# Kernel optimization log

Hardware: AMD Instinct MI355X
Metric: run time of the kernel (lower is better)

Reference implementation:

```python
import jax, jax.numpy as jnp
import numpy as np

B, F, T, K = 16, 256, 2048, 20
TEMP = 0.5
EPS = 1e-8  # torch cosine_similarity eps


def setup_inputs() -> dict:
    key = jax.random.key(0)
    k1, k2, k3 = jax.random.split(key, 3)
    z = jax.random.normal(k1, (B, F, T), dtype=jnp.float32)
    c = jax.random.normal(k2, (B, F, T + 1), dtype=jnp.float32)
    # torch: torch.randint(0, full_len - 1, size=(B, T * K))  -> values in [0, T-2]
    negative_inds = jax.random.randint(k3, (B, T * K), 0, T - 1, dtype=jnp.int64)
    return {"z": z, "c": c, "negative_inds": negative_inds}


def reference(z, c, negative_inds):
    # ---- _generate_negatives ----
    # z: [B, F, T] -> flat rows [B*T, F]
    z_flat = jnp.transpose(z, (0, 2, 1)).reshape(-1, F)
    # per-batch offset i*T (torch adds it in-place for i in 1..B-1)
    inds = negative_inds + (jnp.arange(B, dtype=negative_inds.dtype) * T)[:, None]
    negatives = z_flat[inds.reshape(-1)].reshape(B, T, K, F)

    # ---- _calculate_similarity ----
    c_t = jnp.transpose(c[..., 1:], (0, 2, 1))[:, :, None, :]  # [B, T, 1, F] (drop start token)
    z_t = jnp.transpose(z, (0, 2, 1))[:, :, None, :]           # [B, T, 1, F]
    neg_is_pos = jnp.all(c_t == negatives, axis=-1)            # [B, T, K]
    targets = jnp.concatenate([c_t, negatives], axis=-2)       # [B, T, K+1, F]

    num = jnp.sum(z_t * targets, axis=-1)                      # [B, T, K+1]
    denom = jnp.maximum(
        jnp.linalg.norm(z_t, axis=-1) * jnp.linalg.norm(targets, axis=-1), EPS
    )
    logits = (num / denom) / TEMP                              # [B, T, K+1]

    # mask negatives that exactly equal the positive (wav2vec2-style)
    pad = jnp.zeros_like(neg_is_pos[..., :1])
    full_mask = jnp.concatenate([pad, neg_is_pos], axis=-1)    # [B, T, K+1]
    logits = jnp.where(full_mask, -jnp.inf, logits)

    return logits.reshape(-1, K + 1)                           # [B*T, K+1]
```

## Files before the change

kernel.cpp:

```cpp
#include <hip/hip_runtime.h>
#include <hip/hip_fp16.h>
#include <math.h>

#define B_ 16
#define F_ 256
#define T_ 2048
#define K_ 20
#define OUTK 21
#define NPAIR 11
#define CTOFF (B_ * T_ * F_ * 2)

typedef _Float16 half2v __attribute__((ext_vector_type(2)));

__device__ __forceinline__ half2v h2(unsigned u) { return __builtin_bit_cast(half2v, u); }
__device__ __forceinline__ float fdot2f(unsigned a, unsigned b, float c) {
#if __has_builtin(__builtin_amdgcn_fdot2)
    return __builtin_amdgcn_fdot2(h2(a), h2(b), c, false);
#else
    half2v x = h2(a), y = h2(b);
    return fmaf((float)x[1], (float)y[1], fmaf((float)x[0], (float)y[0], c));
#endif
}

__global__ __launch_bounds__(256) void transpose_norm2_kernel(
    const float* __restrict__ z, const float* __restrict__ c,
    ushort* __restrict__ zth, ushort* __restrict__ cth,
    float* __restrict__ snz, float* __restrict__ snc)
{
    __shared__ float tile[256][33];
    int which = blockIdx.z;
    const float* src = which ? c : z;
    ushort* dst = which ? cth : zth;
    float* nrm = which ? snc : snz;
    int Lsrc = which ? (T_ + 1) : T_;
    int co   = which;

    int b  = blockIdx.y;
    int t0 = blockIdx.x * 32;
    const float* srcb = src + (size_t)b * F_ * Lsrc;
    int tl = threadIdx.x & 31;
    int fl = threadIdx.x >> 5;
#pragma unroll
    for (int i = 0; i < 32; ++i) {
        int f = i * 8 + fl;
        tile[f][tl] = srcb[(size_t)f * Lsrc + (t0 + tl + co)];
    }
    __syncthreads();
    int l   = threadIdx.x & 127;
    int rhi = threadIdx.x >> 7;
#pragma unroll
    for (int j2 = 0; j2 < 16; ++j2) {
        int row = j2 * 2 + rhi;
        float a  = tile[2 * l][row];
        float bb = tile[2 * l + 1][row];
        unsigned u = ((unsigned)__half_as_ushort(__float2half(bb)) << 16)
                   |  (unsigned)__half_as_ushort(__float2half(a));
        unsigned* drow = (unsigned*)(dst + ((size_t)b * T_ + t0 + row) * F_);
        drow[l] = u;
    }
    if (threadIdx.x < 32) {
        float s = 0.f;
#pragma unroll 8
        for (int f = 0; f < 256; ++f) { float v = tile[f][threadIdx.x]; s += v * v; }
        nrm[b * T_ + t0 + threadIdx.x] = sqrtf(s);
    }
}

__device__ __forceinline__ float dpp_half_sum(float x) {
    x += __int_as_float(__builtin_amdgcn_mov_dpp(__float_as_int(x), 0x111, 0xF, 0xF, true));
    x += __int_as_float(__builtin_amdgcn_mov_dpp(__float_as_int(x), 0x112, 0xF, 0xF, true));
    x += __int_as_float(__builtin_amdgcn_mov_dpp(__float_as_int(x), 0x114, 0xF, 0xF, true));
    x += __int_as_float(__builtin_amdgcn_mov_dpp(__float_as_int(x), 0x118, 0xF, 0xF, true));
    x += __int_as_float(__builtin_amdgcn_mov_dpp(__float_as_int(x), 0x142, 0xF, 0xF, true));
    return x;
}

__global__ __launch_bounds__(256, 4) void sim_kernel(
    const ushort* __restrict__ zth, const ushort* __restrict__ cth,
    const float* __restrict__ snz, const float* __restrict__ snc,
    const int* __restrict__ inds, float* __restrict__ out)
{
    __shared__ float sd[128];
    int i = blockIdx.x;
    int b = (i & 7) | ((i >= 4096) ? 8 : 0);
    int wid = threadIdx.x >> 6;
    int t = (((i >> 3) & 511) << 2) + wid;
    int lane = threadIdx.x & 63;
    int hl = lane & 31;
    int hi = lane >> 5;
    int bt = __builtin_amdgcn_readfirstlane((b << 11) + t);

    const int* myinds = inds + bt * K_;
    int idxv = myinds[(lane < K_) ? lane : 0];
    int lm1 = (lane >= 1 && lane <= K_) ? (lane - 1) : 0;
    int myidx = myinds[lm1];
    const float* np = (lane == 0) ? (snc + bt)
                    : ((lane <= K_) ? (snz + ((b << 11) + myidx)) : (snz + bt));
    float stn = *np;
    float szn = snz[bt];

    const uint4* zrow = (const uint4*)(zth + (size_t)bt * F_);
    const uint4* crow = (const uint4*)(cth + (size_t)bt * F_);
    uint4 zv = zrow[hl];
    uint4 cv = crow[hl];

    const char* tbl = (const char*)zth;
    unsigned base_z  = (unsigned)(b << 11) * 512u;
    unsigned laneoff = (unsigned)hl * 16u;

    uint4 tv[NPAIR];
    {
        unsigned olo = (unsigned)CTOFF + (unsigned)bt * 512u;
        unsigned ohi = base_z + (unsigned)__builtin_amdgcn_readlane(idxv, 0) * 512u;
        tv[0] = *(const uint4*)(tbl + ((hi ? ohi : olo) + laneoff));
    }
#pragma unroll
    for (int p = 1; p < NPAIR; ++p) {
        unsigned ilo = (unsigned)__builtin_amdgcn_readlane(idxv, 2 * p - 1);
        unsigned ihi = (unsigned)__builtin_amdgcn_readlane(idxv, (p == 10) ? 19 : 2 * p);
        unsigned off = base_z + (hi ? ihi : ilo) * 512u + laneoff;
        tv[p] = *(const uint4*)(tbl + off);
    }

    __builtin_amdgcn_sched_barrier(0);

    float dz[NPAIR];
#pragma unroll
    for (int p = 0; p < NPAIR; ++p) {
        float d = fdot2f(tv[p].x, zv.x, 0.f);
        d = fdot2f(tv[p].y, zv.y, d);
        d = fdot2f(tv[p].z, zv.z, d);
        d = fdot2f(tv[p].w, zv.w, d);
        dz[p] = d;
    }

    unsigned mb = 0;
#pragma unroll
    for (int p = 0; p < NPAIR; ++p) {
        unsigned long long ball = __ballot(tv[p].x == cv.x);
        unsigned blo = (unsigned)ball, bhi = (unsigned)(ball >> 32);
        if (blo == 0xFFFFFFFFu || bhi == 0xFFFFFFFFu) {
            bool full = (tv[p].x == cv.x) && (tv[p].y == cv.y) &&
                        (tv[p].z == cv.z) && (tv[p].w == cv.w);
            unsigned long long b2 = __ballot(full);
            if ((unsigned)b2 == 0xFFFFFFFFu)          mb |= 1u << (2 * p);
            if ((unsigned)(b2 >> 32) == 0xFFFFFFFFu)  mb |= 1u << (2 * p + 1);
        }
    }
    mb &= ~1u;

#pragma unroll
    for (int p = 0; p < NPAIR; ++p) dz[p] = dpp_half_sum(dz[p]);

    int slotbase = wid * 32 + hi;
    if (hl == 31) {
#pragma unroll
        for (int p = 0; p < NPAIR; ++p) sd[slotbase + 2 * p] = dz[p];
    }

    if (lane < OUTK) {
        float d = sd[wid * 32 + lane];
        float den = fmaxf(szn * stn, 1e-8f);
        float v = (d / den) * 2.0f;
        if ((mb >> lane) & 1u) v = -INFINITY;
        out[(size_t)bt * OUTK + lane] = v;
    }
}

extern "C" void kernel_launch(void* const* d_in, const int* in_sizes, int n_in,
                              void* d_out, int out_size, void* d_ws, size_t ws_size,
                              hipStream_t stream)
{
    const float* z    = (const float*)d_in[0];
    const float* c    = (const float*)d_in[1];
    const int*   inds = (const int*)d_in[2];
    float* out = (float*)d_out;

    char* ws = (char*)d_ws;
    size_t th_bytes = (size_t)B_ * T_ * F_ * sizeof(ushort);
    ushort* zth = (ushort*)ws;
    ushort* cth = (ushort*)(ws + th_bytes);
    float*  snz = (float*)(ws + 2 * th_bytes);
    float*  snc = snz + B_ * T_;

    dim3 tb(256), tg(T_ / 32, B_, 2);
    transpose_norm2_kernel<<<tg, tb, 0, stream>>>(z, c, zth, cth, snz, snc);
    sim_kernel<<<dim3(B_ * T_ / 4), dim3(256), 0, stream>>>(zth, cth, snz, snc, inds, out);
}
```

Baseline: 47.47 us.

## Compute per-row dot products with MFMA 16x16x32 instead of fdot2 plus DPP reduction

Replaces the per-lane fdot2 dot products, DPP cross-lane reduction and LDS staging with two MFMA 16x16x32 f16 ops per K-slice. The anchor z row is replicated as the A operand and 16+5 target rows form the B columns, so each result comes out directly in the accumulator. The equality mask is now built with a cheap first-chunk check and a full compare only when a candidate matches. The A operand re-reads the same row eight times per wave, most of the MFMA output is wasted, and register pressure grows, so the occupancy hint drops from 4 to 3.

```diff
diff --git a/kernel.cpp b/kernel.cpp
--- a/kernel.cpp
+++ b/kernel.cpp
@@ -7,20 +7,10 @@
 #define T_ 2048
 #define K_ 20
 #define OUTK 21
-#define NPAIR 11
 #define CTOFF (B_ * T_ * F_ * 2)
 
-typedef _Float16 half2v __attribute__((ext_vector_type(2)));
-
-__device__ __forceinline__ half2v h2(unsigned u) { return __builtin_bit_cast(half2v, u); }
-__device__ __forceinline__ float fdot2f(unsigned a, unsigned b, float c) {
-#if __has_builtin(__builtin_amdgcn_fdot2)
-    return __builtin_amdgcn_fdot2(h2(a), h2(b), c, false);
-#else
-    half2v x = h2(a), y = h2(b);
-    return fmaf((float)x[1], (float)y[1], fmaf((float)x[0], (float)y[0], c));
-#endif
-}
+typedef _Float16 half8 __attribute__((ext_vector_type(8)));
+typedef float f32x4 __attribute__((ext_vector_type(4)));
 
 __global__ __launch_bounds__(256) void transpose_norm2_kernel(
     const float* __restrict__ z, const float* __restrict__ c,
@@ -66,32 +56,30 @@
     }
 }
 
-__device__ __forceinline__ float dpp_half_sum(float x) {
-    x += __int_as_float(__builtin_amdgcn_mov_dpp(__float_as_int(x), 0x111, 0xF, 0xF, true));
-    x += __int_as_float(__builtin_amdgcn_mov_dpp(__float_as_int(x), 0x112, 0xF, 0xF, true));
-    x += __int_as_float(__builtin_amdgcn_mov_dpp(__float_as_int(x), 0x114, 0xF, 0xF, true));
-    x += __int_as_float(__builtin_amdgcn_mov_dpp(__float_as_int(x), 0x118, 0xF, 0xF, true));
-    x += __int_as_float(__builtin_amdgcn_mov_dpp(__float_as_int(x), 0x142, 0xF, 0xF, true));
-    return x;
+__device__ __forceinline__ unsigned fold16(unsigned long long x) {
+    return (unsigned)(x & 0xFFFFu) & (unsigned)((x >> 16) & 0xFFFFu)
+         & (unsigned)((x >> 32) & 0xFFFFu) & (unsigned)(x >> 48);
+}
+__device__ __forceinline__ bool eq16(uint4 a, uint4 b) {
+    return (a.x == b.x) && (a.y == b.y) && (a.z == b.z) && (a.w == b.w);
 }
 
-__global__ __launch_bounds__(256, 4) void sim_kernel(
+__global__ __launch_bounds__(256, 3) void sim_kernel(
     const ushort* __restrict__ zth, const ushort* __restrict__ cth,
     const float* __restrict__ snz, const float* __restrict__ snc,
     const int* __restrict__ inds, float* __restrict__ out)
 {
-    __shared__ float sd[128];
     int i = blockIdx.x;
     int b = (i & 7) | ((i >= 4096) ? 8 : 0);
     int wid = threadIdx.x >> 6;
     int t = (((i >> 3) & 511) << 2) + wid;
     int lane = threadIdx.x & 63;
-    int hl = lane & 31;
-    int hi = lane >> 5;
+    int slot = lane & 15;
+    int kg = lane >> 4;
     int bt = __builtin_amdgcn_readfirstlane((b << 11) + t);
 
     const int* myinds = inds + bt * K_;
-    int idxv = myinds[(lane < K_) ? lane : 0];
+
     int lm1 = (lane >= 1 && lane <= K_) ? (lane - 1) : 0;
     int myidx = myinds[lm1];
     const float* np = (lane == 0) ? (snc + bt)
@@ -99,67 +87,61 @@
     float stn = *np;
     float szn = snz[bt];
 
-    const uint4* zrow = (const uint4*)(zth + (size_t)bt * F_);
-    const uint4* crow = (const uint4*)(cth + (size_t)bt * F_);
-    uint4 zv = zrow[hl];
-    uint4 cv = crow[hl];
+    int i0 = myinds[(slot >= 1) ? (slot - 1) : 0];
+    int i1 = myinds[(slot <= 4) ? (15 + slot) : 19];
+    unsigned zbase = (unsigned)(b << 11) * 512u;
+    unsigned cbyte = (unsigned)CTOFF + (unsigned)bt * 512u;
+    unsigned rb0 = (slot == 0) ? cbyte : (zbase + (unsigned)i0 * 512u);
+    unsigned rb1 = zbase + (unsigned)i1 * 512u;
+    unsigned qoff = (unsigned)kg * 16u;
+    unsigned abase = (unsigned)bt * 512u;
 
     const char* tbl = (const char*)zth;
-    unsigned base_z  = (unsigned)(b << 11) * 512u;
-    unsigned laneoff = (unsigned)hl * 16u;
 
-    uint4 tv[NPAIR];
-    {
-        unsigned olo = (unsigned)CTOFF + (unsigned)bt * 512u;
-        unsigned ohi = base_z + (unsigned)__builtin_amdgcn_readlane(idxv, 0) * 512u;
-        tv[0] = *(const uint4*)(tbl + ((hi ? ohi : olo) + laneoff));
+    uint4 Bf0[8], Bf1[8], Af[8], c0;
+#pragma unroll
+    for (int s = 0; s < 8; ++s) {
+        Bf0[s] = *(const uint4*)(tbl + rb0 + 64u * s + qoff);
+        Bf1[s] = *(const uint4*)(tbl + rb1 + 64u * s + qoff);
+        Af[s]  = *(const uint4*)(tbl + abase + 64u * s + qoff);
     }
-#pragma unroll
-    for (int p = 1; p < NPAIR; ++p) {
-        unsigned ilo = (unsigned)__builtin_amdgcn_readlane(idxv, 2 * p - 1);
-        unsigned ihi = (unsigned)__builtin_amdgcn_readlane(idxv, (p == 10) ? 19 : 2 * p);
-        unsigned off = base_z + (hi ? ihi : ilo) * 512u + laneoff;
-        tv[p] = *(const uint4*)(tbl + off);
-    }
+    c0 = *(const uint4*)(tbl + cbyte + qoff);
 
     __builtin_amdgcn_sched_barrier(0);
 
-    float dz[NPAIR];
+    f32x4 acc0 = {0.f, 0.f, 0.f, 0.f};
+    f32x4 acc1 = {0.f, 0.f, 0.f, 0.f};
 #pragma unroll
-    for (int p = 0; p < NPAIR; ++p) {
-        float d = fdot2f(tv[p].x, zv.x, 0.f);
-        d = fdot2f(tv[p].y, zv.y, d);
-        d = fdot2f(tv[p].z, zv.z, d);
-        d = fdot2f(tv[p].w, zv.w, d);
-        dz[p] = d;
+    for (int s = 0; s < 8; ++s) {
+        half8 a = __builtin_bit_cast(half8, Af[s]);
+        acc0 = __builtin_amdgcn_mfma_f32_16x16x32_f16(
+                   a, __builtin_bit_cast(half8, Bf0[s]), acc0, 0, 0, 0);
+        acc1 = __builtin_amdgcn_mfma_f32_16x16x32_f16(
+                   a, __builtin_bit_cast(half8, Bf1[s]), acc1, 0, 0, 0);
     }
 
+    bool e0 = eq16(Bf0[0], c0);
+    bool e1 = eq16(Bf1[0], c0);
+    unsigned m0 = fold16(__ballot(e0)) & 0xFFFEu;
+    unsigned m1 = fold16(__ballot(e1)) & 0x001Fu;
     unsigned mb = 0;
+    if (m0 | m1) {
+        bool f0 = e0, f1 = e1;
 #pragma unroll
-    for (int p = 0; p < NPAIR; ++p) {
-        unsigned long long ball = __ballot(tv[p].x == cv.x);
-        unsigned blo = (unsigned)ball, bhi = (unsigned)(ball >> 32);
-        if (blo == 0xFFFFFFFFu || bhi == 0xFFFFFFFFu) {
-            bool full = (tv[p].x == cv.x) && (tv[p].y == cv.y) &&
-                        (tv[p].z == cv.z) && (tv[p].w == cv.w);
-            unsigned long long b2 = __ballot(full);
-            if ((unsigned)b2 == 0xFFFFFFFFu)          mb |= 1u << (2 * p);
-            if ((unsigned)(b2 >> 32) == 0xFFFFFFFFu)  mb |= 1u << (2 * p + 1);
+        for (int s = 1; s < 8; ++s) {
+            uint4 cs = *(const uint4*)(tbl + cbyte + 64u * s + qoff);
+            f0 = f0 && eq16(Bf0[s], cs);
+            f1 = f1 && eq16(Bf1[s], cs);
         }
-    }
-    mb &= ~1u;
-
-#pragma unroll
-    for (int p = 0; p < NPAIR; ++p) dz[p] = dpp_half_sum(dz[p]);
-
-    int slotbase = wid * 32 + hi;
-    if (hl == 31) {
-#pragma unroll
-        for (int p = 0; p < NPAIR; ++p) sd[slotbase + 2 * p] = dz[p];
+        unsigned fm0 = fold16(__ballot(f0)) & 0xFFFEu;
+        unsigned fm1 = fold16(__ballot(f1)) & 0x001Fu;
+        mb = fm0 | (fm1 << 16);
     }
 
+    float d1 = __shfl(acc1[0], lane & 15);
+    float d  = (lane < 16) ? acc0[0] : d1;
+
     if (lane < OUTK) {
-        float d = sd[wid * 32 + lane];
         float den = fmaxf(szn * stn, 1e-8f);
         float v = (d / den) * 2.0f;
         if ((mb >> lane) & 1u) v = -INFINITY;
```

Result: slower. 85.91 us (+81.0%).
